# Kernel optimization log

Measured on AMD Instinct MI355X. Metric: run time of the kernel, lower is better.

## Reference

```python
import jax, jax.numpy as jnp
import numpy as np
import math

B, S, H, HN, D = 4, 1024, 1024, 16, 64  # batch, seq, hidden, heads, head_dim

def setup_inputs() -> dict:
    key = jax.random.key(0)
    ks = jax.random.split(key, 12)
    w = lambda k, shp: (jax.random.normal(k, shp, dtype=jnp.float32) * 0.02)
    return {
        "key": jax.random.normal(ks[0], (B, S, H), dtype=jnp.float32),
        "value": jax.random.normal(ks[1], (B, S, H), dtype=jnp.float32),
        "query": jax.random.normal(ks[2], (B, S, H), dtype=jnp.float32),
        "mask": jnp.zeros((B, 1, S, S), dtype=jnp.float32),
        "position_bias": jax.random.normal(ks[3], (1, HN, S, S), dtype=jnp.float32),
        "prev_attn": jax.random.normal(ks[4], (B, HN, S, S), dtype=jnp.float32),
        "Wq": w(ks[5], (H, HN * D)), "bq": jnp.zeros((HN * D,), jnp.float32),
        "Wk": w(ks[6], (H, HN * D)), "bk": jnp.zeros((HN * D,), jnp.float32),
        "Wv": w(ks[7], (H, HN * D)), "bv": jnp.zeros((HN * D,), jnp.float32),
        "Wo": w(ks[8], (HN * D, H)), "bo": jnp.zeros((H,), jnp.float32),
    }

def reference(key, value, query, mask, position_bias, prev_attn,
              Wq, bq, Wk, bk, Wv, bv, Wo, bo):
    b, s, _ = query.shape
    # QKV projections -> [b, heads, s, d]
    q = (query @ Wq + bq).reshape(b, s, HN, D).transpose(0, 2, 1, 3)
    k = (key @ Wk + bk).reshape(b, s, HN, D).transpose(0, 2, 1, 3)
    v = (value @ Wv + bv).reshape(b, s, HN, D).transpose(0, 2, 1, 3)
    scores = jnp.einsum('bhqd,bhkd->bhqk', q, k)
    # note: position_bias is added BEFORE the 1/sqrt(d) scaling, as in the source
    scores = (scores + position_bias) / math.sqrt(float(D))
    scores = scores + mask
    scores = scores + prev_attn  # has_residual_attention=True path
    prev_attn_out = scores
    probs = jax.nn.softmax(scores, axis=-1)  # dropout p=0.0 -> identity
    ctx = jnp.einsum('bhqk,bhkd->bqhd', probs, v).reshape(b, s, HN * D)
    output = ctx @ Wo + bo
    return (output, prev_attn_out)
```

## Files before the change

kernel.cpp:

```cpp
#include <hip/hip_runtime.h>
#include <hip/hip_bf16.h>
#include <cstdint>

typedef unsigned short u16;
typedef unsigned int u32;

#define BB   4
#define SSQ  1024
#define HHD  1024
#define HNN  16
#define DDIM 64
#define MM   (BB*SSQ)
#define OUT0_ELEMS ((size_t)MM*HHD)
#define SLP  68
#define GST  56

typedef __attribute__((ext_vector_type(8))) short  short8;
typedef __attribute__((ext_vector_type(8))) __bf16 bf16x8;
typedef __attribute__((ext_vector_type(4))) float  f32x4;
typedef __attribute__((ext_vector_type(4))) u16    u16x4;

__device__ __forceinline__ u16 f2b(float f) {
    u32 u = __builtin_bit_cast(u32, f);
    u += 0x7FFFu + ((u >> 16) & 1u);
    return (u16)(u >> 16);
}
__device__ __forceinline__ bf16x8 ld8(const u16* p) {
    return *(const bf16x8*)p;
}
__device__ __forceinline__ f32x4 ldnt4(const float* p) {
    return __builtin_nontemporal_load((const f32x4*)p);
}
__device__ __forceinline__ f32x4 mfma16(bf16x8 a, bf16x8 b, f32x4 c) {
    return __builtin_amdgcn_mfma_f32_16x16x32_bf16(a, b, c, 0, 0, 0);
}

__global__ void conv_wt(const float* __restrict__ w0, const float* __restrict__ w1,
                        const float* __restrict__ w2, const float* __restrict__ w3,
                        u16* __restrict__ out) {
    __shared__ float t[32][33];
    int z = blockIdx.z;
    const float* src = (z == 0) ? w0 : (z == 1) ? w1 : (z == 2) ? w2 : w3;
    int k0 = blockIdx.y * 32, n0 = blockIdx.x * 32;
    int tx = threadIdx.x, ty = threadIdx.y;
    for (int i = ty; i < 32; i += 8)
        t[i][tx] = src[(size_t)(k0 + i) * HHD + n0 + tx];
    __syncthreads();
    u16* dst = out + (size_t)z * HHD * HHD;
    for (int i = ty; i < 32; i += 8)
        dst[(size_t)(n0 + i) * HHD + k0 + tx] = f2b(t[tx][i]);
}

__global__ __launch_bounds__(256) void gemm_xw(
        const float* __restrict__ query, const float* __restrict__ key,
        const float* __restrict__ value, const u16* __restrict__ Wt,
        const float* __restrict__ bq, const float* __restrict__ bk,
        const float* __restrict__ bv,
        u16* __restrict__ qh, u16* __restrict__ kh, u16* __restrict__ vt) {
    __shared__ u16 As[128 * GST];
    __shared__ u16 Bs[128 * GST];
    int z = blockIdx.z;
    const float* Xf = (z == 0) ? query : (z == 1) ? key : value;
    const u16* W = Wt + (size_t)z * HHD * HHD;
    const float* bias = (z == 0) ? bq : (z == 1) ? bk : bv;
    int tid = threadIdx.x;
    int lane = tid & 63, w = tid >> 6;
    int wm = w >> 1, wn = w & 1;
    int rbase = blockIdx.y * 128, cbase = blockIdx.x * 128;
    int lr = lane & 15, lg = lane >> 4;
    int rowb0 = tid >> 2, qb0 = tid & 3;
    int rowb1 = (tid + 256) >> 2, qb1 = tid & 3;
    f32x4 acc[4][4] = {};
    for (int k0 = 0; k0 < HHD; k0 += 32) {
        f32x4 xa[4];
#pragma unroll
        for (int s = 0; s < 4; ++s) {
            int c = tid + s * 256;
            int row = c >> 3, qq = c & 7;
            xa[s] = *(const f32x4*)(Xf + (size_t)(rbase + row) * HHD + k0 + qq * 4);
        }
        f32x4 rb0 = *(const f32x4*)(W + (size_t)(cbase + rowb0) * HHD + k0 + qb0 * 8);
        f32x4 rb1 = *(const f32x4*)(W + (size_t)(cbase + rowb1) * HHD + k0 + qb1 * 8);
        __syncthreads();
#pragma unroll
        for (int s = 0; s < 4; ++s) {
            int c = tid + s * 256;
            int row = c >> 3, qq = c & 7;
            u16x4 o;
#pragma unroll
            for (int e = 0; e < 4; e++) o[e] = f2b(xa[s][e]);
            *(u16x4*)(&As[row * GST + qq * 4]) = o;
        }
        *(f32x4*)(&Bs[rowb0 * GST + qb0 * 8]) = rb0;
        *(f32x4*)(&Bs[rowb1 * GST + qb1 * 8]) = rb1;
        __syncthreads();
        bf16x8 a[4], b[4];
#pragma unroll
        for (int i = 0; i < 4; i++)
            a[i] = *(const bf16x8*)(&As[(wm * 64 + i * 16 + lr) * GST + lg * 8]);
#pragma unroll
        for (int j = 0; j < 4; j++)
            b[j] = *(const bf16x8*)(&Bs[(wn * 64 + j * 16 + lr) * GST + lg * 8]);
#pragma unroll
        for (int i = 0; i < 4; i++)
#pragma unroll
            for (int j = 0; j < 4; j++)
                acc[i][j] = mfma16(a[i], b[j], acc[i][j]);
    }
    int rw = rbase + wm * 64, cw = cbase + wn * 64;
#pragma unroll
    for (int i = 0; i < 4; i++)
#pragma unroll
        for (int j = 0; j < 4; j++) {
            int col = cw + j * 16 + lr;
            float bval = bias[col];
            int h = col >> 6, d = col & 63;
#pragma unroll
            for (int e = 0; e < 4; e++) {
                int row = rw + i * 16 + lg * 4 + e;
                int bidx = row >> 10, s = row & 1023;
                u16 o = f2b(acc[i][j][e] + bval);
                if (z == 0)
                    qh[(((size_t)bidx * HNN + h) * SSQ + s) * DDIM + d] = o;
                else if (z == 1)
                    kh[(((size_t)bidx * HNN + h) * SSQ + s) * DDIM + d] = o;
                else
                    vt[(((size_t)bidx * HNN + h) * DDIM + d) * SSQ + s] = o;
            }
        }
}

__global__ __launch_bounds__(256) void attn_fused(
        const u16* __restrict__ qh, const u16* __restrict__ kh,
        const u16* __restrict__ vt,
        const float* __restrict__ pb, const float* __restrict__ mask,
        const float* __restrict__ prev,
        float* __restrict__ out_sc, u16* __restrict__ ctx) {
    __shared__ float slw[4 * 16 * SLP];
    __shared__ u16   pfw[4 * 16 * 64];
    __shared__ float lsw[64];
    int bh = blockIdx.y;
    int b = bh >> 4, h = bh & 15;
    int rbase0 = blockIdx.x * 64;
    int tid = threadIdx.x, lane = tid & 63, w = tid >> 6;
    int lr = lane & 15, lg = lane >> 4;
    int wr = w * 16;

    const u16* Q = qh + (size_t)bh * SSQ * DDIM;
    const u16* K = kh + (size_t)bh * SSQ * DDIM;
    const u16* V = vt + (size_t)bh * DDIM * SSQ;
    const float* pbh = pb + (size_t)h * SSQ * SSQ;
    const float* mb  = mask + (size_t)b * SSQ * SSQ;
    const float* pr  = prev + (size_t)bh * SSQ * SSQ;
    float* ob = out_sc + (size_t)bh * SSQ * SSQ;

    float* ws = slw + w * 16 * SLP;
    char* pslice = (char*)pfw + w * 2048;

    bf16x8 aq[2];
#pragma unroll
    for (int ks = 0; ks < 2; ks++)
        aq[ks] = ld8(Q + (size_t)(rbase0 + wr + lr) * DDIM + ks * 32 + lg * 8);

    f32x4 acc_pv[4] = {};
    float seacc[4] = {0.f, 0.f, 0.f, 0.f};

    for (int kt = 0; kt < 16; ++kt) {
        int cb = kt * 64;
        size_t eidx = (size_t)(rbase0 + wr + lg) * SSQ + cb + lr * 4;
        f32x4 pF = *(const f32x4*)(pbh + eidx);
        f32x4 mF = *(const f32x4*)(mb + eidx);
        f32x4 rF = ldnt4(pr + eidx);
        bf16x8 bv[4][2];
#pragma unroll
        for (int j = 0; j < 4; j++)
#pragma unroll
            for (int ks = 0; ks < 2; ks++)
                bv[j][ks] = ld8(V + (size_t)(j * 16 + lr) * SSQ + cb + ks * 32 + lg * 8);
        bf16x8 bk[4][2];
#pragma unroll
        for (int j = 0; j < 4; j++)
#pragma unroll
            for (int ks = 0; ks < 2; ks++)
                bk[j][ks] = ld8(K + (size_t)(cb + j * 16 + lr) * DDIM + ks * 32 + lg * 8);
        f32x4 acc_s[4] = {};
        __builtin_amdgcn_s_setprio(1);
#pragma unroll
        for (int ks = 0; ks < 2; ks++)
#pragma unroll
            for (int j = 0; j < 4; j++)
                acc_s[j] = mfma16(aq[ks], bk[j][ks], acc_s[j]);
        __builtin_amdgcn_s_setprio(0);
#pragma unroll
        for (int j = 0; j < 4; j++)
#pragma unroll
            for (int e = 0; e < 4; e++)
                ws[(lg * 4 + e) * SLP + j * 16 + lr] = acc_s[j][e];

#pragma unroll
        for (int it = 0; it < 4; ++it) {
            int rl = it * 4 + lg;
            size_t idx = (size_t)(rbase0 + wr + rl) * SSQ + cb + lr * 4;
            f32x4 p4 = pF, m4 = mF, r4 = rF;
            if (it < 3) {
                size_t idx2 = idx + (size_t)4 * SSQ;
                pF = *(const f32x4*)(pbh + idx2);
                mF = *(const f32x4*)(mb + idx2);
                rF = ldnt4(pr + idx2);
            }
            f32x4 s4 = *(const f32x4*)(ws + rl * SLP + lr * 4);
            f32x4 o4;
#pragma unroll
            for (int c = 0; c < 4; c++)
                o4[c] = (s4[c] + p4[c]) * 0.125f + m4[c] + r4[c];
            __builtin_nontemporal_store(o4, (f32x4*)(ob + idx));
            f32x4 e4;
#pragma unroll
            for (int c = 0; c < 4; c++) e4[c] = __expf(o4[c]);
            u16x4 pk;
#pragma unroll
            for (int c = 0; c < 4; c++) pk[c] = f2b(e4[c]);
            int byte = (rl * 128 + lr * 8) ^ ((rl & 7) << 4);
            *(u16x4*)(pslice + byte) = pk;
            float se = e4[0] + e4[1] + e4[2] + e4[3];
#pragma unroll
            for (int off = 8; off >= 1; off >>= 1) se += __shfl_xor(se, off);
            seacc[it] += se;
        }

        bf16x8 a[2];
#pragma unroll
        for (int ks = 0; ks < 2; ks++) {
            int byte = (lr * 128 + ks * 64 + lg * 16) ^ ((lr & 7) << 4);
            a[ks] = *(const bf16x8*)(pslice + byte);
        }
        __builtin_amdgcn_s_setprio(1);
#pragma unroll
        for (int j = 0; j < 4; j++)
#pragma unroll
            for (int ks = 0; ks < 2; ks++)
                acc_pv[j] = mfma16(a[ks], bv[j][ks], acc_pv[j]);
        __builtin_amdgcn_s_setprio(0);
    }

    if (lr == 0) {
#pragma unroll
        for (int it = 0; it < 4; ++it)
            lsw[wr + it * 4 + lg] = seacc[it];
    }
    float linv[4];
#pragma unroll
    for (int e = 0; e < 4; e++)
        linv[e] = 1.f / lsw[wr + lg * 4 + e];
#pragma unroll
    for (int j = 0; j < 4; j++) {
        int d = j * 16 + lr;
#pragma unroll
        for (int e = 0; e < 4; e++) {
            int row = rbase0 + wr + lg * 4 + e;
            ctx[((size_t)(b * SSQ + row)) * HHD + h * DDIM + d] =
                f2b(acc_pv[j][e] * linv[e]);
        }
    }
}

__global__ __launch_bounds__(256) void gemm_out(
        const u16* __restrict__ ctxb, const u16* __restrict__ WtO,
        const float* __restrict__ bo, float* __restrict__ out) {
    __shared__ u16 As[128 * GST];
    __shared__ u16 Bs[128 * GST];
    int tid = threadIdx.x;
    int lane = tid & 63, w = tid >> 6;
    int wm = w >> 1, wn = w & 1;
    int rbase = blockIdx.y * 128, cbase = blockIdx.x * 128;
    int lr = lane & 15, lg = lane >> 4;
    int row0 = tid >> 2, q0 = tid & 3;
    int row1 = (tid + 256) >> 2, q1 = tid & 3;
    f32x4 acc[4][4] = {};
    for (int k0 = 0; k0 < HHD; k0 += 32) {
        f32x4 ra0 = *(const f32x4*)(ctxb + (size_t)(rbase + row0) * HHD + k0 + q0 * 8);
        f32x4 rb0 = *(const f32x4*)(WtO + (size_t)(cbase + row0) * HHD + k0 + q0 * 8);
        f32x4 ra1 = *(const f32x4*)(ctxb + (size_t)(rbase + row1) * HHD + k0 + q1 * 8);
        f32x4 rb1 = *(const f32x4*)(WtO + (size_t)(cbase + row1) * HHD + k0 + q1 * 8);
        __syncthreads();
        *(f32x4*)(&As[row0 * GST + q0 * 8]) = ra0;
        *(f32x4*)(&Bs[row0 * GST + q0 * 8]) = rb0;
        *(f32x4*)(&As[row1 * GST + q1 * 8]) = ra1;
        *(f32x4*)(&Bs[row1 * GST + q1 * 8]) = rb1;
        __syncthreads();
        bf16x8 a[4], b[4];
#pragma unroll
        for (int i = 0; i < 4; i++)
            a[i] = *(const bf16x8*)(&As[(wm * 64 + i * 16 + lr) * GST + lg * 8]);
#pragma unroll
        for (int j = 0; j < 4; j++)
            b[j] = *(const bf16x8*)(&Bs[(wn * 64 + j * 16 + lr) * GST + lg * 8]);
#pragma unroll
        for (int i = 0; i < 4; i++)
#pragma unroll
            for (int j = 0; j < 4; j++)
                acc[i][j] = mfma16(a[i], b[j], acc[i][j]);
    }
    int rw = rbase + wm * 64, cw = cbase + wn * 64;
#pragma unroll
    for (int i = 0; i < 4; i++)
#pragma unroll
        for (int j = 0; j < 4; j++) {
            int col = cw + j * 16 + lr;
            float bval = bo[col];
#pragma unroll
            for (int e = 0; e < 4; e++) {
                int row = rw + i * 16 + lg * 4 + e;
                out[(size_t)row * HHD + col] = acc[i][j][e] + bval;
            }
        }
}

extern "C" void kernel_launch(void* const* d_in, const int* in_sizes, int n_in,
                              void* d_out, int out_size, void* d_ws, size_t ws_size,
                              hipStream_t stream) {
    const float* key   = (const float*)d_in[0];
    const float* value = (const float*)d_in[1];
    const float* query = (const float*)d_in[2];
    const float* mask  = (const float*)d_in[3];
    const float* pb    = (const float*)d_in[4];
    const float* prev  = (const float*)d_in[5];
    const float* Wq    = (const float*)d_in[6];
    const float* bq    = (const float*)d_in[7];
    const float* Wk    = (const float*)d_in[8];
    const float* bk    = (const float*)d_in[9];
    const float* Wv    = (const float*)d_in[10];
    const float* bv    = (const float*)d_in[11];
    const float* Wo    = (const float*)d_in[12];
    const float* bo    = (const float*)d_in[13];

    u16* Wt  = (u16*)d_ws;
    u16* qh  = Wt + (size_t)4 * HHD * HHD;
    u16* kh  = qh + (size_t)MM * HHD;
    u16* vt  = kh + (size_t)MM * HHD;
    u16* ctx = vt + (size_t)MM * HHD;

    float* out0 = (float*)d_out;
    float* sc   = out0 + OUT0_ELEMS;

    conv_wt<<<dim3(32, 32, 4), dim3(32, 8), 0, stream>>>(Wq, Wk, Wv, Wo, Wt);
    gemm_xw<<<dim3(8, 32, 3), 256, 0, stream>>>(query, key, value, Wt, bq, bk, bv, qh, kh, vt);
    attn_fused<<<dim3(16, 64), 256, 0, stream>>>(qh, kh, vt, pb, mask, prev, sc, ctx);
    gemm_out<<<dim3(8, 32), 256, 0, stream>>>(ctx, Wt + (size_t)3 * HHD * HHD, bo, out0);
}
```

Baseline: 315.4 us.

## Widen attention key tile to 128 columns and reuse score LDS for probabilities

The fused attention loop now processes 128 key columns per iteration instead of 64, halving the outer iteration count. Each elementwise pass covers two rows of 128 columns per wave, so every row's global loads are 512 contiguous bytes. The bf16 probabilities are written in place over the fp32 score buffer, which removes the separate swizzled probability buffer and its XOR swizzle. This aims to improve global coalescing and amortise loop overhead, at the cost of more shared memory per block, more live registers and possible LDS bank conflicts without the swizzle.

After: 313.7 us. No clear change (-0.5%).

```diff
diff --git a/kernel.cpp b/kernel.cpp
--- a/kernel.cpp
+++ b/kernel.cpp
@@ -12,7 +12,7 @@
 #define DDIM 64
 #define MM   (BB*SSQ)
 #define OUT0_ELEMS ((size_t)MM*HHD)
-#define SLP  68
+#define SLP2 130
 #define GST  56
 
 typedef __attribute__((ext_vector_type(8))) short  short8;
@@ -136,14 +136,14 @@
         const float* __restrict__ pb, const float* __restrict__ mask,
         const float* __restrict__ prev,
         float* __restrict__ out_sc, u16* __restrict__ ctx) {
-    __shared__ float slw[4 * 16 * SLP];
-    __shared__ u16   pfw[4 * 16 * 64];
+    __shared__ float slw[4 * 16 * SLP2];
     __shared__ float lsw[64];
     int bh = blockIdx.y;
     int b = bh >> 4, h = bh & 15;
     int rbase0 = blockIdx.x * 64;
     int tid = threadIdx.x, lane = tid & 63, w = tid >> 6;
     int lr = lane & 15, lg = lane >> 4;
+    int c4 = lane & 31, hg = lane >> 5;
     int wr = w * 16;
 
     const u16* Q = qh + (size_t)bh * SSQ * DDIM;
@@ -154,8 +154,8 @@
     const float* pr  = prev + (size_t)bh * SSQ * SSQ;
     float* ob = out_sc + (size_t)bh * SSQ * SSQ;
 
-    float* ws = slw + w * 16 * SLP;
-    char* pslice = (char*)pfw + w * 2048;
+    float* ws = slw + w * 16 * SLP2;
+    char* wsb = (char*)ws;
 
     bf16x8 aq[2];
 #pragma unroll
@@ -163,52 +163,51 @@
         aq[ks] = ld8(Q + (size_t)(rbase0 + wr + lr) * DDIM + ks * 32 + lg * 8);
 
     f32x4 acc_pv[4] = {};
-    float seacc[4] = {0.f, 0.f, 0.f, 0.f};
-
-    for (int kt = 0; kt < 16; ++kt) {
-        int cb = kt * 64;
-        size_t eidx = (size_t)(rbase0 + wr + lg) * SSQ + cb + lr * 4;
+    float seacc[8] = {0.f, 0.f, 0.f, 0.f, 0.f, 0.f, 0.f, 0.f};
+
+    for (int kt = 0; kt < 8; ++kt) {
+        int cb = kt * 128;
+        size_t eidx = (size_t)(rbase0 + wr + hg) * SSQ + cb + c4 * 4;
         f32x4 pF = *(const f32x4*)(pbh + eidx);
         f32x4 mF = *(const f32x4*)(mb + eidx);
         f32x4 rF = ldnt4(pr + eidx);
-        bf16x8 bv[4][2];
-#pragma unroll
-        for (int j = 0; j < 4; j++)
+
+#pragma unroll
+        for (int half = 0; half < 2; ++half) {
+            int cbh = cb + half * 64;
+            bf16x8 bk[4][2];
+#pragma unroll
+            for (int j = 0; j < 4; j++)
+#pragma unroll
+                for (int ks = 0; ks < 2; ks++)
+                    bk[j][ks] = ld8(K + (size_t)(cbh + j * 16 + lr) * DDIM + ks * 32 + lg * 8);
+            f32x4 acc_s[4] = {};
+            __builtin_amdgcn_s_setprio(1);
 #pragma unroll
             for (int ks = 0; ks < 2; ks++)
-                bv[j][ks] = ld8(V + (size_t)(j * 16 + lr) * SSQ + cb + ks * 32 + lg * 8);
-        bf16x8 bk[4][2];
-#pragma unroll
-        for (int j = 0; j < 4; j++)
-#pragma unroll
-            for (int ks = 0; ks < 2; ks++)
-                bk[j][ks] = ld8(K + (size_t)(cb + j * 16 + lr) * DDIM + ks * 32 + lg * 8);
-        f32x4 acc_s[4] = {};
-        __builtin_amdgcn_s_setprio(1);
-#pragma unroll
-        for (int ks = 0; ks < 2; ks++)
-#pragma unroll
-            for (int j = 0; j < 4; j++)
-                acc_s[j] = mfma16(aq[ks], bk[j][ks], acc_s[j]);
-        __builtin_amdgcn_s_setprio(0);
-#pragma unroll
-        for (int j = 0; j < 4; j++)
-#pragma unroll
-            for (int e = 0; e < 4; e++)
-                ws[(lg * 4 + e) * SLP + j * 16 + lr] = acc_s[j][e];
-
-#pragma unroll
-        for (int it = 0; it < 4; ++it) {
-            int rl = it * 4 + lg;
-            size_t idx = (size_t)(rbase0 + wr + rl) * SSQ + cb + lr * 4;
+#pragma unroll
+                for (int j = 0; j < 4; j++)
+                    acc_s[j] = mfma16(aq[ks], bk[j][ks], acc_s[j]);
+            __builtin_amdgcn_s_setprio(0);
+#pragma unroll
+            for (int j = 0; j < 4; j++)
+#pragma unroll
+                for (int e = 0; e < 4; e++)
+                    ws[(lg * 4 + e) * SLP2 + half * 64 + j * 16 + lr] = acc_s[j][e];
+        }
+
+#pragma unroll
+        for (int it = 0; it < 8; ++it) {
+            int rl = it * 2 + hg;
+            size_t idx = (size_t)(rbase0 + wr + rl) * SSQ + cb + c4 * 4;
             f32x4 p4 = pF, m4 = mF, r4 = rF;
-            if (it < 3) {
-                size_t idx2 = idx + (size_t)4 * SSQ;
+            if (it < 7) {
+                size_t idx2 = idx + (size_t)2 * SSQ;
                 pF = *(const f32x4*)(pbh + idx2);
                 mF = *(const f32x4*)(mb + idx2);
                 rF = ldnt4(pr + idx2);
             }
-            f32x4 s4 = *(const f32x4*)(ws + rl * SLP + lr * 4);
+            f32x4 s4 = *(const f32x4*)(ws + rl * SLP2 + c4 * 4);
             f32x4 o4;
 #pragma unroll
             for (int c = 0; c < 4; c++)
@@ -220,33 +219,43 @@
             u16x4 pk;
 #pragma unroll
             for (int c = 0; c < 4; c++) pk[c] = f2b(e4[c]);
-            int byte = (rl * 128 + lr * 8) ^ ((rl & 7) << 4);
-            *(u16x4*)(pslice + byte) = pk;
+            *(u16x4*)(wsb + rl * (SLP2 * 4) + c4 * 8) = pk;
             float se = e4[0] + e4[1] + e4[2] + e4[3];
 #pragma unroll
-            for (int off = 8; off >= 1; off >>= 1) se += __shfl_xor(se, off);
+            for (int off = 16; off >= 1; off >>= 1) se += __shfl_xor(se, off);
             seacc[it] += se;
         }
 
-        bf16x8 a[2];
-#pragma unroll
-        for (int ks = 0; ks < 2; ks++) {
-            int byte = (lr * 128 + ks * 64 + lg * 16) ^ ((lr & 7) << 4);
-            a[ks] = *(const bf16x8*)(pslice + byte);
-        }
-        __builtin_amdgcn_s_setprio(1);
-#pragma unroll
-        for (int j = 0; j < 4; j++)
-#pragma unroll
-            for (int ks = 0; ks < 2; ks++)
-                acc_pv[j] = mfma16(a[ks], bv[j][ks], acc_pv[j]);
-        __builtin_amdgcn_s_setprio(0);
-    }
-
-    if (lr == 0) {
-#pragma unroll
-        for (int it = 0; it < 4; ++it)
-            lsw[wr + it * 4 + lg] = seacc[it];
+#pragma unroll
+        for (int half = 0; half < 2; ++half) {
+            bf16x8 a2[2];
+#pragma unroll
+            for (int kk = 0; kk < 2; kk++) {
+                int ks = half * 2 + kk;
+                a2[kk] = *(const bf16x8*)(wsb + lr * (SLP2 * 4) + ks * 64 + lg * 16);
+            }
+            bf16x8 bv2[4][2];
+#pragma unroll
+            for (int j = 0; j < 4; j++)
+#pragma unroll
+                for (int kk = 0; kk < 2; kk++) {
+                    int ks = half * 2 + kk;
+                    bv2[j][kk] = ld8(V + (size_t)(j * 16 + lr) * SSQ + cb + ks * 32 + lg * 8);
+                }
+            __builtin_amdgcn_s_setprio(1);
+#pragma unroll
+            for (int j = 0; j < 4; j++)
+#pragma unroll
+                for (int kk = 0; kk < 2; kk++)
+                    acc_pv[j] = mfma16(a2[kk], bv2[j][kk], acc_pv[j]);
+            __builtin_amdgcn_s_setprio(0);
+        }
+    }
+
+    if (c4 == 0) {
+#pragma unroll
+        for (int it = 0; it < 8; ++it)
+            lsw[wr + it * 2 + hg] = seacc[it];
     }
     float linv[4];
 #pragma unroll
```
